# Optimization experiments

Measured on AMD Instinct MI355X. Metric: run time of the kernel, lower is better.

## Reference

```python
import jax, jax.numpy as jnp
import numpy as np

V, H, DEPTH = 32000, 512, 6
B, L = 8, 256
AD, TD = 1024, 1024
TA, TT = 200, 100
DI, DS, DC, DTR = 1024, 16, 4, 32  # d_inner=2*H, d_state, d_conv, dt_rank=ceil(H/16)


def causal_conv1d(x, w, b):
    # x: [B,L,DI], w: [DI,DC], b: [DI]; depthwise causal conv
    K = w.shape[1]
    xp = jnp.pad(x, ((0, 0), (K - 1, 0), (0, 0)))
    out = b
    for k in range(K):
        out = out + xp[:, k:k + x.shape[1], :] * w[:, k]
    return out


def layernorm(x, g, b, eps=1e-5):
    mu = jnp.mean(x, -1, keepdims=True)
    var = jnp.var(x, -1, keepdims=True)
    return (x - mu) * jax.lax.rsqrt(var + eps) * g + b


def mamba_block(x, ipw, cw, cb, xpw, dtw, dtb, Alog, Dp, ow):
    # x: [B,L,H]
    xz = x @ ipw.T                       # [B,L,2*DI]
    xin, z = jnp.split(xz, 2, axis=-1)
    xc = jax.nn.silu(causal_conv1d(xin, cw, cb))  # [B,L,DI]
    dbl = xc @ xpw.T                     # [B,L,DTR+2*DS]
    dt = jax.nn.softplus(dbl[..., :DTR] @ dtw.T + dtb)    # [B,L,DI]
    Bm = dbl[..., DTR:DTR + DS]          # [B,L,DS]
    Cm = dbl[..., DTR + DS:]             # [B,L,DS]
    A = -jnp.exp(Alog)                   # [DI,DS]
    dA = jnp.exp(dt[..., None] * A)                       # [B,L,DI,DS]
    dBu = dt[..., None] * Bm[:, :, None, :] * xc[..., None]

    def step(h, inp):
        dA_t, dBu_t, C_t = inp
        h = h * dA_t + dBu_t             # [B,DI,DS]
        return h, jnp.einsum('bds,bs->bd', h, C_t)

    h0 = jnp.zeros((x.shape[0], DI, DS), x.dtype)
    _, ys = jax.lax.scan(step, h0, (dA.transpose(1, 0, 2, 3),
                                    dBu.transpose(1, 0, 2, 3),
                                    Cm.transpose(1, 0, 2)))
    y = ys.transpose(1, 0, 2) + Dp * xc  # [B,L,DI]
    y = y * jax.nn.silu(z)
    return y @ ow.T                      # [B,L,H]


def setup_inputs() -> dict:
    key = jax.random.key(0)
    ks = jax.random.split(key, 32)
    f = jnp.float32
    s = 0.02
    inp = {
        'input_ids': jax.random.randint(ks[0], (B, L), 0, V),
        'audio_feats': jax.random.normal(ks[1], (B, TA, AD), f),
        'text_feats': jax.random.normal(ks[2], (B, TT, TD), f),
        'audio_mask': jnp.zeros((B, TA), bool),
        'text_mask': jnp.zeros((B, TT), bool),
        'tok_emb': jax.random.normal(ks[3], (V, H), f) * s,
        'pos_emb': jax.random.normal(ks[4], (1, L, H), f) * s,
        'audio_w': jax.random.normal(ks[5], (H, AD), f) * s,
        'audio_b': jnp.zeros((H,), f),
        'text_w': jax.random.normal(ks[6], (H, TD), f) * s,
        'text_b': jnp.zeros((H,), f),
        'mod_emb': jnp.zeros((2, H), f),
        'cond_w': jax.random.normal(ks[7], (H, H), f) * s,
        'cond_b': jnp.zeros((H,), f),
        'in_proj_w': jax.random.normal(ks[8], (DEPTH, 2 * DI, H), f) * s,
        'conv_w': jax.random.normal(ks[9], (DEPTH, DI, DC), f) * s,
        'conv_b': jnp.zeros((DEPTH, DI), f),
        'x_proj_w': jax.random.normal(ks[10], (DEPTH, DTR + 2 * DS, DI), f) * s,
        'dt_w': jax.random.normal(ks[11], (DEPTH, DI, DTR), f) * s,
        'dt_b': jnp.full((DEPTH, DI), -4.6, f),  # softplus(-4.6)~0.01, realistic dt init
        'A_log': jnp.broadcast_to(jnp.log(jnp.arange(1, DS + 1, dtype=f)), (DEPTH, DI, DS)) + 0.0,
        'D_skip': jnp.ones((DEPTH, DI), f),
        'out_w': jax.random.normal(ks[12], (DEPTH, H, DI), f) * s,
        'ln_g': jnp.ones((DEPTH, H), f),
        'ln_b': jnp.zeros((DEPTH, H), f),
        'head_w': jax.random.normal(ks[13], (V, H), f) * s,
        'head_b': jnp.zeros((V,), f),
    }
    return inp


def reference(input_ids, audio_feats, text_feats, audio_mask, text_mask,
              tok_emb, pos_emb, audio_w, audio_b, text_w, text_b, mod_emb,
              cond_w, cond_b, in_proj_w, conv_w, conv_b, x_proj_w, dt_w, dt_b,
              A_log, D_skip, out_w, ln_g, ln_b, head_w, head_b):
    x = tok_emb[input_ids] + pos_emb[:, :input_ids.shape[1], :]
    # build memory + pooled condition
    mem_a = audio_feats @ audio_w.T + audio_b + mod_emb[0]
    mem_t = text_feats @ text_w.T + text_b + mod_emb[1]
    memory = jnp.concatenate([mem_a, mem_t], axis=1)      # [B,TA+TT,H]
    mask = jnp.concatenate([audio_mask, text_mask], axis=1)
    valid = (~mask)[..., None].astype(memory.dtype)
    denom = jnp.maximum(valid.sum(axis=1), 1.0)
    pooled = (memory * valid).sum(axis=1) / denom
    cond = pooled @ cond_w.T + cond_b
    x = x + cond[:, None, :]
    for i in range(DEPTH):
        y = mamba_block(x, in_proj_w[i], conv_w[i], conv_b[i], x_proj_w[i],
                        dt_w[i], dt_b[i], A_log[i], D_skip[i], out_w[i])
        x = layernorm(x + y, ln_g[i], ln_b[i])
    return x @ head_w.T + head_b  # [B,L,V]
```

## Files before the change

### kernel.cpp

```cpp
#include <hip/hip_runtime.h>
#include <hip/hip_bf16.h>

#define V_    32000
#define H_    512
#define DEPTH_ 6
#define B_    8
#define L_    256
#define TA_   200
#define TT_   100
#define AD_   1024
#define DI_   1024
#define DS_   16
#define DTR_  32
#define M_    (B_*L_)

typedef __hip_bfloat16 bf16;
static __device__ __forceinline__ float b2f(bf16 x){ return __bfloat162float(x); }
static __device__ __forceinline__ float siluf(float x){ return x / (1.f + __expf(-x)); }

template<bool F32>
static __device__ __forceinline__ float ld(const void* p, size_t i){
    if (F32) return ((const float*)p)[i];
    else     return __bfloat162float(((const bf16*)p)[i]);
}

typedef __attribute__((ext_vector_type(8))) short s16x8;
typedef __attribute__((ext_vector_type(4))) float f32x4;

static __device__ __forceinline__ short f2bf_s(float f){
    union { bf16 b; short s; } u; u.b = __float2bfloat16(f); return u.s;
}
static __device__ __forceinline__ float bf_s2f(short s){
    union { bf16 b; short s2; } u; u.s2 = s; return __bfloat162float(u.b);
}
static __device__ __forceinline__ void split2(float f, short &h, short &l){
    h = f2bf_s(f);
    l = f2bf_s(f - bf_s2f(h));
}

__global__ void detect_kernel(const bf16* __restrict__ tok, int* __restrict__ flag){
    __shared__ int s;
    if (threadIdx.x==0) s = 0;
    __syncthreads();
    for (int i=threadIdx.x; i<4096; i+=256){
        float v = b2f(tok[i]);
        if (!(fabsf(v) < 1e3f)) atomicOr(&s, 1);
    }
    __syncthreads();
    if (threadIdx.x==0) *flag = s;
}

template<bool F32>
__global__ void feat_sum_kernel(const void* __restrict__ feats, const unsigned char* __restrict__ mask,
                                int T, float* __restrict__ out, const int* __restrict__ fl)
{
    if ((*fl!=0)!=F32) return;
    int d = blockIdx.x*256 + threadIdx.x;
    int b = blockIdx.y;
    const unsigned char* mb = mask + b*T;
    float s = 0.f;
    for (int t=0;t<T;t++) if (!mb[t]) s += ld<F32>(feats, (size_t)b*T*AD_ + (size_t)t*AD_ + d);
    out[b*AD_+d] = s;
}

__global__ void count_kernel(const unsigned char* __restrict__ am, const unsigned char* __restrict__ tm,
                             float* __restrict__ cnt )
{
    int i = threadIdx.x;
    if (i < B_)        { int c=0; for (int t=0;t<TA_;t++) c += am[i*TA_+t]?0:1; cnt[i] = (float)c; }
    else if (i < 2*B_) { int b=i-B_; int c=0; for (int t=0;t<TT_;t++) c += tm[b*TT_+t]?0:1; cnt[B_+b]=(float)c; }
}

template<bool F32>
__global__ __launch_bounds__(256) void pooled_kernel(const float* __restrict__ sa, const float* __restrict__ st,
    const float* __restrict__ cnt, const void* __restrict__ Wa, const void* __restrict__ ab,
    const void* __restrict__ Wt, const void* __restrict__ tb, const void* __restrict__ me,
    float* __restrict__ pooled, const int* __restrict__ fl)
{
    if ((*fl!=0)!=F32) return;
    int b = blockIdx.x;
    __shared__ float s_a[AD_], s_t[AD_];
    for (int i=threadIdx.x;i<AD_;i+=256){ s_a[i]=sa[b*AD_+i]; s_t[i]=st[b*AD_+i]; }
    __syncthreads();
    float ca = cnt[b], ct = cnt[B_+b];
    float denom = fmaxf(ca+ct, 1.0f);
    for (int h=threadIdx.x; h<H_; h+=256){
        float acc = 0.f;
        for (int k=0;k<AD_;k++) acc = fmaf(s_a[k], ld<F32>(Wa,(size_t)h*AD_+k), acc);
        for (int k=0;k<AD_;k++) acc = fmaf(s_t[k], ld<F32>(Wt,(size_t)h*AD_+k), acc);
        acc += ca*(ld<F32>(ab,h) + ld<F32>(me,h));
        acc += ct*(ld<F32>(tb,h) + ld<F32>(me,H_+h));
        pooled[b*H_+h] = acc/denom;
    }
}

template<bool F32>
__global__ __launch_bounds__(256) void cond_kernel(const float* __restrict__ pooled,
    const void* __restrict__ cw, const void* __restrict__ cb, float* __restrict__ cond,
    const int* __restrict__ fl)
{
    if ((*fl!=0)!=F32) return;
    int b = blockIdx.x;
    __shared__ float ps[H_];
    for (int i=threadIdx.x;i<H_;i+=256) ps[i]=pooled[b*H_+i];
    __syncthreads();
    for (int h=threadIdx.x; h<H_; h+=256){
        float acc = ld<F32>(cb,h);
        for (int k=0;k<H_;k++) acc = fmaf(ps[k], ld<F32>(cw,(size_t)h*H_+k), acc);
        cond[b*H_+h] = acc;
    }
}

template<bool F32>
__global__ void embed_kernel(const int* __restrict__ ids, const void* __restrict__ tok,
    const void* __restrict__ pos, const float* __restrict__ cond, float* __restrict__ x,
    const int* __restrict__ fl)
{
    if ((*fl!=0)!=F32) return;
    int tid = blockIdx.x*256 + threadIdx.x;
    if (tid >= M_*H_) return;
    int m = tid >> 9, h = tid & (H_-1);
    int b = m >> 8, l = m & (L_-1);
    x[tid] = ld<F32>(tok,(size_t)ids[m]*H_ + h) + ld<F32>(pos,(size_t)l*H_+h) + cond[b*H_+h];
}

template<bool F32>
__global__ __launch_bounds__(256) void gemm_kernel(const float* __restrict__ A, const void* __restrict__ Bw,
    float* __restrict__ Cf, void* __restrict__ Cb, const void* __restrict__ bias,
    int M, int N, int K, int MLOOP, const int* __restrict__ fl)
{
    if ((*fl!=0)!=F32) return;
    __shared__ short Ah[128][40];
    __shared__ short Al[128][40];
    __shared__ short Bh[128][40];
    __shared__ short Bl[128][40];

    const int tid = threadIdx.x;
    const int l    = tid & 63;
    const int wid  = tid >> 6;
    const int wr   = wid >> 1, wc = wid & 1;
    const int lrow = l & 15;
    const int lk   = (l >> 4) << 3;
    const int n0   = blockIdx.x * 128;

    for (int mt = 0; mt < MLOOP; ++mt){
        const int m0 = (blockIdx.y * MLOOP + mt) * 128;
        f32x4 acc[4][4] = {};

        for (int k0 = 0; k0 < K; k0 += 32){
            #pragma unroll
            for (int p=0;p<4;p++){
                int fidx = (p<<8) + tid;
                int row  = fidx >> 3;
                int kq   = (fidx & 7) << 2;
                float4 v = *(const float4*)(A + (size_t)(m0+row)*K + k0 + kq);
                short4 h, lo;
                split2(v.x, h.x, lo.x);
                split2(v.y, h.y, lo.y);
                split2(v.z, h.z, lo.z);
                split2(v.w, h.w, lo.w);
                *(short4*)&Ah[row][kq] = h;
                *(short4*)&Al[row][kq] = lo;
            }
            if (F32){
                #pragma unroll
                for (int p=0;p<4;p++){
                    int fidx = (p<<8) + tid;
                    int row  = fidx >> 3;
                    int kq   = (fidx & 7) << 2;
                    float4 v = *(const float4*)((const float*)Bw + (size_t)(n0+row)*K + k0 + kq);
                    short4 h, lo;
                    split2(v.x, h.x, lo.x);
                    split2(v.y, h.y, lo.y);
                    split2(v.z, h.z, lo.z);
                    split2(v.w, h.w, lo.w);
                    *(short4*)&Bh[row][kq] = h;
                    *(short4*)&Bl[row][kq] = lo;
                }
            } else {
                #pragma unroll
                for (int p=0;p<2;p++){
                    int fidx = (p<<8) + tid;
                    int row  = fidx >> 2;
                    int kq   = (fidx & 3) << 3;
                    s16x8 v = *(const s16x8*)((const short*)Bw + (size_t)(n0+row)*K + k0 + kq);
                    *(s16x8*)&Bh[row][kq] = v;
                }
            }
            __syncthreads();

            s16x8 fah[4], fal[4], fbh[4], fbl[4];
            #pragma unroll
            for (int i=0;i<4;i++){
                int ar = wr*64 + i*16 + lrow;
                fah[i] = *(const s16x8*)&Ah[ar][lk];
                fal[i] = *(const s16x8*)&Al[ar][lk];
                int br = wc*64 + i*16 + lrow;
                fbh[i] = *(const s16x8*)&Bh[br][lk];
                if (F32) fbl[i] = *(const s16x8*)&Bl[br][lk];
            }
            #pragma unroll
            for (int i=0;i<4;i++){
                #pragma unroll
                for (int j=0;j<4;j++){
                    acc[i][j] = __builtin_amdgcn_mfma_f32_16x16x32_bf16(fah[i], fbh[j], acc[i][j], 0,0,0);
                    acc[i][j] = __builtin_amdgcn_mfma_f32_16x16x32_bf16(fal[i], fbh[j], acc[i][j], 0,0,0);
                    if (F32)
                        acc[i][j] = __builtin_amdgcn_mfma_f32_16x16x32_bf16(fah[i], fbl[j], acc[i][j], 0,0,0);
                }
            }
            __syncthreads();
        }

        const int rbase = (l >> 4) << 2;
        #pragma unroll
        for (int i=0;i<4;i++){
            int mrow = m0 + wr*64 + i*16 + rbase;
            #pragma unroll
            for (int j=0;j<4;j++){
                int ncol = n0 + wc*64 + j*16 + lrow;
                float bv = bias ? ld<F32>(bias,(size_t)ncol) : 0.f;
                #pragma unroll
                for (int r=0;r<4;r++){
                    float outv = acc[i][j][r] + bv;
                    if (Cb){
                        if (F32) ((float*)Cb)[(size_t)(mrow+r)*N+ncol] = outv;
                        else     ((bf16*)Cb)[(size_t)(mrow+r)*N+ncol] = __float2bfloat16(outv);
                    } else {
                        Cf[(size_t)(mrow+r)*N+ncol] = outv;
                    }
                }
            }
        }
    }
}

template<bool F32>
__global__ void conv_silu_kernel(const float* __restrict__ xz, const void* __restrict__ cw,
                                 const void* __restrict__ cb, float* __restrict__ xc,
                                 const int* __restrict__ fl)
{
    if ((*fl!=0)!=F32) return;
    int tid = blockIdx.x*256 + threadIdx.x;
    if (tid >= M_*DI_) return;
    int m = tid >> 10, d = tid & (DI_-1);
    int l = m & (L_-1);
    float acc = ld<F32>(cb,d);
    #pragma unroll
    for (int k=0;k<4;k++){
        int l2 = l - 3 + k;
        if (l2 >= 0) acc = fmaf(xz[(size_t)(m-3+k)*(2*DI_) + d], ld<F32>(cw,(size_t)d*4+k), acc);
    }
    xc[tid] = siluf(acc);
}

template<bool F32>
__global__ __launch_bounds__(256) void xproj_kernel(const float* __restrict__ xc,
    const void* __restrict__ xpw, float* __restrict__ dbl, const int* __restrict__ fl)
{
    if ((*fl!=0)!=F32) return;
    int m = blockIdx.x;
    __shared__ float xs[DI_];
    __shared__ float part[64][5];
    for (int i=threadIdx.x;i<DI_;i+=256) xs[i] = xc[(size_t)m*DI_ + i];
    __syncthreads();
    int n = threadIdx.x & 63, c = threadIdx.x >> 6;
    const float* xv = xs + c*256;
    size_t wo = (size_t)n*DI_ + c*256;
    float acc = 0.f;
    for (int k=0;k<256;k++) acc = fmaf(xv[k], ld<F32>(xpw, wo+k), acc);
    part[n][c] = acc;
    __syncthreads();
    if (threadIdx.x < 64){
        dbl[(size_t)m*64 + threadIdx.x] = part[threadIdx.x][0]+part[threadIdx.x][1]
                                        + part[threadIdx.x][2]+part[threadIdx.x][3];
    }
}

template<bool F32>
__global__ __launch_bounds__(256) void dt_kernel(const float* __restrict__ dbl, const void* __restrict__ dtw,
    const void* __restrict__ dtb, float* __restrict__ dt, const int* __restrict__ fl)
{
    if ((*fl!=0)!=F32) return;
    int tid = blockIdx.x*256 + threadIdx.x;
    int m = tid >> 10;
    int d = tid & (DI_-1);
    __shared__ float ds_[DTR_];
    if (threadIdx.x < DTR_) ds_[threadIdx.x] = dbl[(size_t)m*64 + threadIdx.x];
    __syncthreads();
    float acc = ld<F32>(dtb,d);
    #pragma unroll
    for (int j=0;j<DTR_;j++) acc = fmaf(ds_[j], ld<F32>(dtw,(size_t)d*DTR_+j), acc);
    float sp = acc > 0.f ? acc + log1pf(__expf(-acc)) : log1pf(__expf(acc));
    dt[tid] = sp;
}

template<bool F32>
__global__ __launch_bounds__(256) void scan_kernel(const float* __restrict__ dt, const float* __restrict__ xc,
    const float* __restrict__ dbl, const float* __restrict__ xz,
    const void* __restrict__ Alog, const void* __restrict__ Dsk,
    float* __restrict__ ys, const int* __restrict__ fl)
{
    if ((*fl!=0)!=F32) return;
    int tid = threadIdx.x;
    int s = tid & 15, dloc = tid >> 4;
    int d = blockIdx.x*16 + dloc;
    int b = blockIdx.y;
    float aA = -__expf(ld<F32>(Alog,(size_t)d*DS_+s));
    float dp = ld<F32>(Dsk,d);
    float h = 0.f;
    int m0 = b*L_;
    float dtc = dt[(size_t)m0*DI_ + d];
    float xcc = xc[(size_t)m0*DI_ + d];
    float Bc  = dbl[(size_t)m0*64 + 32 + s];
    float Cc  = dbl[(size_t)m0*64 + 48 + s];
    for (int t=0;t<L_;t++){
        int m  = m0 + t;
        int mn = m + (t < L_-1 ? 1 : 0);
        float dtn = dt[(size_t)mn*DI_ + d];
        float xcn = xc[(size_t)mn*DI_ + d];
        float Bn  = dbl[(size_t)mn*64 + 32 + s];
        float Cn  = dbl[(size_t)mn*64 + 48 + s];
        float dA = __expf(dtc * aA);
        h = fmaf(h, dA, dtc*Bc*xcc);
        float p = h*Cc;
        p += __shfl_xor(p, 1, 16);
        p += __shfl_xor(p, 2, 16);
        p += __shfl_xor(p, 4, 16);
        p += __shfl_xor(p, 8, 16);
        if (s == 0){
            float zv = xz[(size_t)m*(2*DI_) + DI_ + d];
            ys[(size_t)m*DI_ + d] = (p + dp*xcc) * siluf(zv);
        }
        dtc=dtn; xcc=xcn; Bc=Bn; Cc=Cn;
    }
}

template<bool F32>
__global__ __launch_bounds__(256) void add_ln_kernel(float* __restrict__ x, const float* __restrict__ yp,
    const void* __restrict__ g, const void* __restrict__ bt, const int* __restrict__ fl)
{
    if ((*fl!=0)!=F32) return;
    int m = blockIdx.x;
    int tid = threadIdx.x;
    float r0 = x[(size_t)m*H_ + tid]       + yp[(size_t)m*H_ + tid];
    float r1 = x[(size_t)m*H_ + tid + 256] + yp[(size_t)m*H_ + tid + 256];
    float s = r0 + r1, q = r0*r0 + r1*r1;
    #pragma unroll
    for (int off=32; off>=1; off>>=1){ s += __shfl_xor(s, off, 64); q += __shfl_xor(q, off, 64); }
    __shared__ float ss[4], qq[4];
    int w = tid >> 6;
    if ((tid & 63)==0){ ss[w]=s; qq[w]=q; }
    __syncthreads();
    float S = ss[0]+ss[1]+ss[2]+ss[3];
    float Q = qq[0]+qq[1]+qq[2]+qq[3];
    float mean = S / (float)H_;
    float var  = Q / (float)H_ - mean*mean;
    float inv  = rsqrtf(var + 1e-5f);
    x[(size_t)m*H_+tid]       = (r0-mean)*inv*ld<F32>(g,tid)     + ld<F32>(bt,tid);
    x[(size_t)m*H_+tid+256]   = (r1-mean)*inv*ld<F32>(g,tid+256) + ld<F32>(bt,tid+256);
}

#define DUAL(kern, grid, block, ...) do { \
    kern<false><<<grid, block, 0, stream>>>(__VA_ARGS__); \
    kern<true><<<grid, block, 0, stream>>>(__VA_ARGS__); } while(0)

extern "C" void kernel_launch(void* const* d_in, const int* in_sizes, int n_in,
                              void* d_out, int out_size, void* d_ws, size_t ws_size,
                              hipStream_t stream)
{
    const int*  ids = (const int*)d_in[0];
    const void* af  = d_in[1];
    const void* tf  = d_in[2];
    const unsigned char* am = (const unsigned char*)d_in[3];
    const unsigned char* tm = (const unsigned char*)d_in[4];
    const void* tok = d_in[5];
    const void* pos = d_in[6];
    const void* aw  = d_in[7];
    const void* ab  = d_in[8];
    const void* tw  = d_in[9];
    const void* tbb = d_in[10];
    const void* me  = d_in[11];
    const void* cw  = d_in[12];
    const void* cb  = d_in[13];
    const void* ipw = d_in[14];
    const void* cvw = d_in[15];
    const void* cvb = d_in[16];
    const void* xpw = d_in[17];
    const void* dtw = d_in[18];
    const void* dtb = d_in[19];
    const void* Alg = d_in[20];
    const void* Dsk = d_in[21];
    const void* ow  = d_in[22];
    const void* lng = d_in[23];
    const void* lnb = d_in[24];
    const void* hw  = d_in[25];
    const void* hb  = d_in[26];

    float* ws   = (float*)d_ws;
    float* x    = ws;
    float* xz   = x    + (size_t)M_*H_;
    float* xc   = xz   + (size_t)M_*2*DI_;
    float* dbl  = xc   + (size_t)M_*DI_;
    float* dtv  = dbl  + (size_t)M_*64;
    float* ysb  = dtv  + (size_t)M_*DI_;
    float* ypj  = ysb  + (size_t)M_*DI_;
    float* sa   = ypj  + (size_t)M_*H_;
    float* st   = sa   + B_*AD_;
    float* cnt  = st   + B_*AD_;
    float* pooled = cnt + 2*B_;
    float* cond = pooled + B_*H_;
    int*   dflag = (int*)(cond + B_*H_);

    detect_kernel<<<1, 256, 0, stream>>>((const bf16*)tok, dflag);

    DUAL(feat_sum_kernel, dim3(AD_/256, B_), 256, af, am, TA_, sa, dflag);
    DUAL(feat_sum_kernel, dim3(AD_/256, B_), 256, tf, tm, TT_, st, dflag);
    count_kernel<<<1, 64, 0, stream>>>(am, tm, cnt);
    DUAL(pooled_kernel, B_, 256, sa, st, cnt, aw, ab, tw, tbb, me, pooled, dflag);
    DUAL(cond_kernel, B_, 256, pooled, cw, cb, cond, dflag);
    DUAL(embed_kernel, (M_*H_+255)/256, 256, ids, tok, pos, cond, x, dflag);

    for (int layer=0; layer<DEPTH_; ++layer){
        size_t o_ipw = (size_t)layer*2*DI_*H_;
        size_t o_cvw = (size_t)layer*DI_*4;
        size_t o_cvb = (size_t)layer*DI_;
        size_t o_xpw = (size_t)layer*64*DI_;
        size_t o_dtw = (size_t)layer*DI_*DTR_;
        size_t o_dtb = (size_t)layer*DI_;
        size_t o_alg = (size_t)layer*DI_*DS_;
        size_t o_dsk = (size_t)layer*DI_;
        size_t o_ow  = (size_t)layer*H_*DI_;
        size_t o_ln  = (size_t)layer*H_;
        const void* ipw_h = (const void*)((const bf16*)ipw + o_ipw);
        const void* ipw_f = (const void*)((const float*)ipw + o_ipw);
        const void* cvw_h = (const void*)((const bf16*)cvw + o_cvw);
        const void* cvw_f = (const void*)((const float*)cvw + o_cvw);
        const void* cvb_h = (const void*)((const bf16*)cvb + o_cvb);
        const void* cvb_f = (const void*)((const float*)cvb + o_cvb);
        const void* xpw_h = (const void*)((const bf16*)xpw + o_xpw);
        const void* xpw_f = (const void*)((const float*)xpw + o_xpw);
        const void* dtw_h = (const void*)((const bf16*)dtw + o_dtw);
        const void* dtw_f = (const void*)((const float*)dtw + o_dtw);
        const void* dtb_h = (const void*)((const bf16*)dtb + o_dtb);
        const void* dtb_f = (const void*)((const float*)dtb + o_dtb);
        const void* alg_h = (const void*)((const bf16*)Alg + o_alg);
        const void* alg_f = (const void*)((const float*)Alg + o_alg);
        const void* dsk_h = (const void*)((const bf16*)Dsk + o_dsk);
        const void* dsk_f = (const void*)((const float*)Dsk + o_dsk);
        const void* ow_h  = (const void*)((const bf16*)ow + o_ow);
        const void* ow_f  = (const void*)((const float*)ow + o_ow);
        const void* lng_h = (const void*)((const bf16*)lng + o_ln);
        const void* lng_f = (const void*)((const float*)lng + o_ln);
        const void* lnb_h = (const void*)((const bf16*)lnb + o_ln);
        const void* lnb_f = (const void*)((const float*)lnb + o_ln);

        gemm_kernel<false><<<dim3(2*DI_/128, M_/128), 256, 0, stream>>>(x, ipw_h, xz, nullptr, nullptr, M_, 2*DI_, H_, 1, dflag);
        gemm_kernel<true ><<<dim3(2*DI_/128, M_/128), 256, 0, stream>>>(x, ipw_f, xz, nullptr, nullptr, M_, 2*DI_, H_, 1, dflag);
        conv_silu_kernel<false><<<(M_*DI_+255)/256, 256, 0, stream>>>(xz, cvw_h, cvb_h, xc, dflag);
        conv_silu_kernel<true ><<<(M_*DI_+255)/256, 256, 0, stream>>>(xz, cvw_f, cvb_f, xc, dflag);
        xproj_kernel<false><<<M_, 256, 0, stream>>>(xc, xpw_h, dbl, dflag);
        xproj_kernel<true ><<<M_, 256, 0, stream>>>(xc, xpw_f, dbl, dflag);
        dt_kernel<false><<<M_*DI_/256, 256, 0, stream>>>(dbl, dtw_h, dtb_h, dtv, dflag);
        dt_kernel<true ><<<M_*DI_/256, 256, 0, stream>>>(dbl, dtw_f, dtb_f, dtv, dflag);
        scan_kernel<false><<<dim3(DI_/16, B_), 256, 0, stream>>>(dtv, xc, dbl, xz, alg_h, dsk_h, ysb, dflag);
        scan_kernel<true ><<<dim3(DI_/16, B_), 256, 0, stream>>>(dtv, xc, dbl, xz, alg_f, dsk_f, ysb, dflag);
        gemm_kernel<false><<<dim3(H_/128, M_/128), 256, 0, stream>>>(ysb, ow_h, ypj, nullptr, nullptr, M_, H_, DI_, 1, dflag);
        gemm_kernel<true ><<<dim3(H_/128, M_/128), 256, 0, stream>>>(ysb, ow_f, ypj, nullptr, nullptr, M_, H_, DI_, 1, dflag);
        add_ln_kernel<false><<<M_, 256, 0, stream>>>(x, ypj, lng_h, lnb_h, dflag);
        add_ln_kernel<true ><<<M_, 256, 0, stream>>>(x, ypj, lng_f, lnb_f, dflag);
    }

    DUAL(gemm_kernel, dim3(V_/128, M_/(128*8)), 256, x, hw, nullptr, d_out, hb, M_, V_, H_, 8, dflag);
}
```

Baseline: 3.305 ms.

## Pre-split activations into bf16 hi/lo, fuse conv/xproj/dt, nontemporal head stores

Producers (embed, add_ln, scan) now write the activations already split into bf16 high and low halves. The GEMMs load these directly instead of re-splitting fp32 A tiles for every output column block. The conv+silu, x_proj and dt/softplus kernels are merged into a single per-row mid kernel, which removes two launch pairs and the intermediate round trips. The final vocab-head GEMM uses nontemporal stores for its large output. In exchange, the hi/lo activation buffers take extra memory, the producers do more writes, and the shared memory for B-low is shrunk in the bf16 path.

```diff
diff --git a/kernel.cpp b/kernel.cpp
--- a/kernel.cpp
+++ b/kernel.cpp
@@ -114,26 +114,31 @@
 template<bool F32>
 __global__ void embed_kernel(const int* __restrict__ ids, const void* __restrict__ tok,
     const void* __restrict__ pos, const float* __restrict__ cond, float* __restrict__ x,
-    const int* __restrict__ fl)
+    short* __restrict__ xh, short* __restrict__ xl, const int* __restrict__ fl)
 {
     if ((*fl!=0)!=F32) return;
     int tid = blockIdx.x*256 + threadIdx.x;
     if (tid >= M_*H_) return;
     int m = tid >> 9, h = tid & (H_-1);
     int b = m >> 8, l = m & (L_-1);
-    x[tid] = ld<F32>(tok,(size_t)ids[m]*H_ + h) + ld<F32>(pos,(size_t)l*H_+h) + cond[b*H_+h];
-}
-
-template<bool F32>
-__global__ __launch_bounds__(256) void gemm_kernel(const float* __restrict__ A, const void* __restrict__ Bw,
+    float v = ld<F32>(tok,(size_t)ids[m]*H_ + h) + ld<F32>(pos,(size_t)l*H_+h) + cond[b*H_+h];
+    x[tid] = v;
+    short hh, ll; split2(v, hh, ll);
+    xh[tid] = hh; xl[tid] = ll;
+}
+
+template<bool F32>
+__global__ __launch_bounds__(256) void gemm_kernel(
+    const short* __restrict__ Ah, const short* __restrict__ Al,
+    const void* __restrict__ Bw,
     float* __restrict__ Cf, void* __restrict__ Cb, const void* __restrict__ bias,
-    int M, int N, int K, int MLOOP, const int* __restrict__ fl)
-{
-    if ((*fl!=0)!=F32) return;
-    __shared__ short Ah[128][40];
-    __shared__ short Al[128][40];
-    __shared__ short Bh[128][40];
-    __shared__ short Bl[128][40];
+    int M, int N, int K, int MLOOP, int NT, const int* __restrict__ fl)
+{
+    if ((*fl!=0)!=F32) return;
+    __shared__ short Ahs[128][40];
+    __shared__ short Als[128][40];
+    __shared__ short Bhs[128][40];
+    __shared__ short Bls[F32?128:1][40];
 
     const int tid = threadIdx.x;
     const int l    = tid & 63;
@@ -149,18 +154,12 @@
 
         for (int k0 = 0; k0 < K; k0 += 32){
             #pragma unroll
-            for (int p=0;p<4;p++){
+            for (int p=0;p<2;p++){
                 int fidx = (p<<8) + tid;
-                int row  = fidx >> 3;
-                int kq   = (fidx & 7) << 2;
-                float4 v = *(const float4*)(A + (size_t)(m0+row)*K + k0 + kq);
-                short4 h, lo;
-                split2(v.x, h.x, lo.x);
-                split2(v.y, h.y, lo.y);
-                split2(v.z, h.z, lo.z);
-                split2(v.w, h.w, lo.w);
-                *(short4*)&Ah[row][kq] = h;
-                *(short4*)&Al[row][kq] = lo;
+                int row  = fidx >> 2;
+                int kq   = (fidx & 3) << 3;
+                *(s16x8*)&Ahs[row][kq] = *(const s16x8*)(Ah + (size_t)(m0+row)*K + k0 + kq);
+                *(s16x8*)&Als[row][kq] = *(const s16x8*)(Al + (size_t)(m0+row)*K + k0 + kq);
             }
             if (F32){
                 #pragma unroll
@@ -174,8 +173,8 @@
                     split2(v.y, h.y, lo.y);
                     split2(v.z, h.z, lo.z);
                     split2(v.w, h.w, lo.w);
-                    *(short4*)&Bh[row][kq] = h;
-                    *(short4*)&Bl[row][kq] = lo;
+                    *(short4*)&Bhs[row][kq] = h;
+                    *(short4*)&Bls[row][kq] = lo;
                 }
             } else {
                 #pragma unroll
@@ -183,8 +182,7 @@
                     int fidx = (p<<8) + tid;
                     int row  = fidx >> 2;
                     int kq   = (fidx & 3) << 3;
-                    s16x8 v = *(const s16x8*)((const short*)Bw + (size_t)(n0+row)*K + k0 + kq);
-                    *(s16x8*)&Bh[row][kq] = v;
+                    *(s16x8*)&Bhs[row][kq] = *(const s16x8*)((const short*)Bw + (size_t)(n0+row)*K + k0 + kq);
                 }
             }
             __syncthreads();
@@ -193,11 +191,11 @@
             #pragma unroll
             for (int i=0;i<4;i++){
                 int ar = wr*64 + i*16 + lrow;
-                fah[i] = *(const s16x8*)&Ah[ar][lk];
-                fal[i] = *(const s16x8*)&Al[ar][lk];
+                fah[i] = *(const s16x8*)&Ahs[ar][lk];
+                fal[i] = *(const s16x8*)&Als[ar][lk];
                 int br = wc*64 + i*16 + lrow;
-                fbh[i] = *(const s16x8*)&Bh[br][lk];
-                if (F32) fbl[i] = *(const s16x8*)&Bl[br][lk];
+                fbh[i] = *(const s16x8*)&Bhs[br][lk];
+                if (F32) fbl[i] = *(const s16x8*)&Bls[br][lk];
             }
             #pragma unroll
             for (int i=0;i<4;i++){
@@ -224,8 +222,16 @@
                 for (int r=0;r<4;r++){
                     float outv = acc[i][j][r] + bv;
                     if (Cb){
-                        if (F32) ((float*)Cb)[(size_t)(mrow+r)*N+ncol] = outv;
-                        else     ((bf16*)Cb)[(size_t)(mrow+r)*N+ncol] = __float2bfloat16(outv);
+                        if (F32){
+                            float* pp = (float*)Cb + (size_t)(mrow+r)*N+ncol;
+                            if (NT) __builtin_nontemporal_store(outv, pp);
+                            else    *pp = outv;
+                        } else {
+                            short sv = f2bf_s(outv);
+                            short* pp = (short*)Cb + (size_t)(mrow+r)*N+ncol;
+                            if (NT) __builtin_nontemporal_store(sv, pp);
+                            else    *pp = sv;
+                        }
                     } else {
                         Cf[(size_t)(mrow+r)*N+ncol] = outv;
                     }
@@ -236,70 +242,65 @@
 }
 
 template<bool F32>
-__global__ void conv_silu_kernel(const float* __restrict__ xz, const void* __restrict__ cw,
-                                 const void* __restrict__ cb, float* __restrict__ xc,
-                                 const int* __restrict__ fl)
-{
-    if ((*fl!=0)!=F32) return;
-    int tid = blockIdx.x*256 + threadIdx.x;
-    if (tid >= M_*DI_) return;
-    int m = tid >> 10, d = tid & (DI_-1);
+__global__ __launch_bounds__(256) void mid_kernel(const float* __restrict__ xz,
+    const void* __restrict__ cw, const void* __restrict__ cb,
+    const void* __restrict__ xpw, const void* __restrict__ dtw, const void* __restrict__ dtb,
+    float* __restrict__ xc, float* __restrict__ dbl, float* __restrict__ dtv,
+    const int* __restrict__ fl)
+{
+    if ((*fl!=0)!=F32) return;
+    int m = blockIdx.x;
     int l = m & (L_-1);
-    float acc = ld<F32>(cb,d);
-    #pragma unroll
-    for (int k=0;k<4;k++){
-        int l2 = l - 3 + k;
-        if (l2 >= 0) acc = fmaf(xz[(size_t)(m-3+k)*(2*DI_) + d], ld<F32>(cw,(size_t)d*4+k), acc);
-    }
-    xc[tid] = siluf(acc);
-}
-
-template<bool F32>
-__global__ __launch_bounds__(256) void xproj_kernel(const float* __restrict__ xc,
-    const void* __restrict__ xpw, float* __restrict__ dbl, const int* __restrict__ fl)
-{
-    if ((*fl!=0)!=F32) return;
-    int m = blockIdx.x;
+    int tid = threadIdx.x;
     __shared__ float xs[DI_];
     __shared__ float part[64][5];
-    for (int i=threadIdx.x;i<DI_;i+=256) xs[i] = xc[(size_t)m*DI_ + i];
-    __syncthreads();
-    int n = threadIdx.x & 63, c = threadIdx.x >> 6;
+    __shared__ float ds_[DTR_];
+
+    #pragma unroll
+    for (int p=0;p<4;p++){
+        int d = tid + (p<<8);
+        float acc = ld<F32>(cb,d);
+        #pragma unroll
+        for (int k=0;k<4;k++){
+            int l2 = l - 3 + k;
+            if (l2 >= 0) acc = fmaf(xz[(size_t)(m-3+k)*(2*DI_) + d], ld<F32>(cw,(size_t)d*4+k), acc);
+        }
+        float v = siluf(acc);
+        xs[d] = v;
+        xc[(size_t)m*DI_ + d] = v;
+    }
+    __syncthreads();
+
+    int n = tid & 63, c = tid >> 6;
     const float* xv = xs + c*256;
     size_t wo = (size_t)n*DI_ + c*256;
     float acc = 0.f;
     for (int k=0;k<256;k++) acc = fmaf(xv[k], ld<F32>(xpw, wo+k), acc);
     part[n][c] = acc;
     __syncthreads();
-    if (threadIdx.x < 64){
-        dbl[(size_t)m*64 + threadIdx.x] = part[threadIdx.x][0]+part[threadIdx.x][1]
-                                        + part[threadIdx.x][2]+part[threadIdx.x][3];
-    }
-}
-
-template<bool F32>
-__global__ __launch_bounds__(256) void dt_kernel(const float* __restrict__ dbl, const void* __restrict__ dtw,
-    const void* __restrict__ dtb, float* __restrict__ dt, const int* __restrict__ fl)
-{
-    if ((*fl!=0)!=F32) return;
-    int tid = blockIdx.x*256 + threadIdx.x;
-    int m = tid >> 10;
-    int d = tid & (DI_-1);
-    __shared__ float ds_[DTR_];
-    if (threadIdx.x < DTR_) ds_[threadIdx.x] = dbl[(size_t)m*64 + threadIdx.x];
-    __syncthreads();
-    float acc = ld<F32>(dtb,d);
+    if (tid < 64){
+        float s = part[tid][0]+part[tid][1]+part[tid][2]+part[tid][3];
+        dbl[(size_t)m*64 + tid] = s;
+        if (tid < DTR_) ds_[tid] = s;
+    }
+    __syncthreads();
+
     #pragma unroll
-    for (int j=0;j<DTR_;j++) acc = fmaf(ds_[j], ld<F32>(dtw,(size_t)d*DTR_+j), acc);
-    float sp = acc > 0.f ? acc + log1pf(__expf(-acc)) : log1pf(__expf(acc));
-    dt[tid] = sp;
+    for (int p=0;p<4;p++){
+        int d = tid + (p<<8);
+        float a2 = ld<F32>(dtb,d);
+        #pragma unroll
+        for (int j=0;j<DTR_;j++) a2 = fmaf(ds_[j], ld<F32>(dtw,(size_t)d*DTR_+j), a2);
+        float sp = a2 > 0.f ? a2 + log1pf(__expf(-a2)) : log1pf(__expf(a2));
+        dtv[(size_t)m*DI_ + d] = sp;
+    }
 }
 
 template<bool F32>
 __global__ __launch_bounds__(256) void scan_kernel(const float* __restrict__ dt, const float* __restrict__ xc,
     const float* __restrict__ dbl, const float* __restrict__ xz,
     const void* __restrict__ Alog, const void* __restrict__ Dsk,
-    float* __restrict__ ys, const int* __restrict__ fl)
+    short* __restrict__ ysh, short* __restrict__ ysl, const int* __restrict__ fl)
 {
     if ((*fl!=0)!=F32) return;
     int tid = threadIdx.x;
@@ -330,7 +331,10 @@
         p += __shfl_xor(p, 8, 16);
         if (s == 0){
             float zv = xz[(size_t)m*(2*DI_) + DI_ + d];
-            ys[(size_t)m*DI_ + d] = (p + dp*xcc) * siluf(zv);
+            float yv = (p + dp*xcc) * siluf(zv);
+            short hh, ll; split2(yv, hh, ll);
+            ysh[(size_t)m*DI_ + d] = hh;
+            ysl[(size_t)m*DI_ + d] = ll;
         }
         dtc=dtn; xcc=xcn; Bc=Bn; Cc=Cn;
     }
@@ -338,7 +342,8 @@
 
 template<bool F32>
 __global__ __launch_bounds__(256) void add_ln_kernel(float* __restrict__ x, const float* __restrict__ yp,
-    const void* __restrict__ g, const void* __restrict__ bt, const int* __restrict__ fl)
+    const void* __restrict__ g, const void* __restrict__ bt,
+    short* __restrict__ xh, short* __restrict__ xl, const int* __restrict__ fl)
 {
     if ((*fl!=0)!=F32) return;
     int m = blockIdx.x;
@@ -357,8 +362,13 @@
     float mean = S / (float)H_;
     float var  = Q / (float)H_ - mean*mean;
     float inv  = rsqrtf(var + 1e-5f);
-    x[(size_t)m*H_+tid]       = (r0-mean)*inv*ld<F32>(g,tid)     + ld<F32>(bt,tid);
-    x[(size_t)m*H_+tid+256]   = (r1-mean)*inv*ld<F32>(g,tid+256) + ld<F32>(bt,tid+256);
+    float o0 = (r0-mean)*inv*ld<F32>(g,tid)     + ld<F32>(bt,tid);
+    float o1 = (r1-mean)*inv*ld<F32>(g,tid+256) + ld<F32>(bt,tid+256);
+    x[(size_t)m*H_+tid]     = o0;
+    x[(size_t)m*H_+tid+256] = o1;
+    short hh, ll;
+    split2(o0, hh, ll); xh[(size_t)m*H_+tid]     = hh; xl[(size_t)m*H_+tid]     = ll;
+    split2(o1, hh, ll); xh[(size_t)m*H_+tid+256] = hh; xl[(size_t)m*H_+tid+256] = ll;
 }
 
 #define DUAL(kern, grid, block, ...) do { \
@@ -410,7 +420,12 @@
     float* cnt  = st   + B_*AD_;
     float* pooled = cnt + 2*B_;
     float* cond = pooled + B_*H_;
-    int*   dflag = (int*)(cond + B_*H_);
+    short* xh   = (short*)(cond + B_*H_);
+    short* xl   = xh + (size_t)M_*H_;
+    int*   dflag = (int*)(xl + (size_t)M_*H_);
+
+    short* ysh  = (short*)ysb;
+    short* ysl  = ysh + (size_t)M_*DI_;
 
     detect_kernel<<<1, 256, 0, stream>>>((const bf16*)tok, dflag);
 
@@ -419,7 +434,7 @@
     count_kernel<<<1, 64, 0, stream>>>(am, tm, cnt);
     DUAL(pooled_kernel, B_, 256, sa, st, cnt, aw, ab, tw, tbb, me, pooled, dflag);
     DUAL(cond_kernel, B_, 256, pooled, cw, cb, cond, dflag);
-    DUAL(embed_kernel, (M_*H_+255)/256, 256, ids, tok, pos, cond, x, dflag);
+    DUAL(embed_kernel, (M_*H_+255)/256, 256, ids, tok, pos, cond, x, xh, xl, dflag);
 
     for (int layer=0; layer<DEPTH_; ++layer){
         size_t o_ipw = (size_t)layer*2*DI_*H_;
@@ -455,21 +470,17 @@
         const void* lnb_h = (const void*)((const bf16*)lnb + o_ln);
         const void* lnb_f = (const void*)((const float*)lnb + o_ln);
 
-        gemm_kernel<false><<<dim3(2*DI_/128, M_/128), 256, 0, stream>>>(x, ipw_h, xz, nullptr, nullptr, M_, 2*DI_, H_, 1, dflag);
-        gemm_kernel<true ><<<dim3(2*DI_/128, M_/128), 256, 0, stream>>>(x, ipw_f, xz, nullptr, nullptr, M_, 2*DI_, H_, 1, dflag);
-        conv_silu_kernel<false><<<(M_*DI_+255)/256, 256, 0, stream>>>(xz, cvw_h, cvb_h, xc, dflag);
-        conv_silu_kernel<true ><<<(M_*DI_+255)/256, 256, 0, stream>>>(xz, cvw_f, cvb_f, xc, dflag);
-        xproj_kernel<false><<<M_, 256, 0, stream>>>(xc, xpw_h, dbl, dflag);
-        xproj_kernel<true ><<<M_, 256, 0, stream>>>(xc, xpw_f, dbl, dflag);
-        dt_kernel<false><<<M_*DI_/256, 256, 0, stream>>>(dbl, dtw_h, dtb_h, dtv, dflag);
-        dt_kernel<true ><<<M_*DI_/256, 256, 0, stream>>>(dbl, dtw_f, dtb_f, dtv, dflag);
-        scan_kernel<false><<<dim3(DI_/16, B_), 256, 0, stream>>>(dtv, xc, dbl, xz, alg_h, dsk_h, ysb, dflag);
-        scan_kernel<true ><<<dim3(DI_/16, B_), 256, 0, stream>>>(dtv, xc, dbl, xz, alg_f, dsk_f, ysb, dflag);
-        gemm_kernel<false><<<dim3(H_/128, M_/128), 256, 0, stream>>>(ysb, ow_h, ypj, nullptr, nullptr, M_, H_, DI_, 1, dflag);
-        gemm_kernel<true ><<<dim3(H_/128, M_/128), 256, 0, stream>>>(ysb, ow_f, ypj, nullptr, nullptr, M_, H_, DI_, 1, dflag);
-        add_ln_kernel<false><<<M_, 256, 0, stream>>>(x, ypj, lng_h, lnb_h, dflag);
-        add_ln_kernel<true ><<<M_, 256, 0, stream>>>(x, ypj, lng_f, lnb_f, dflag);
-    }
-
-    DUAL(gemm_kernel, dim3(V_/128, M_/(128*8)), 256, x, hw, nullptr, d_out, hb, M_, V_, H_, 8, dflag);
-}
+        gemm_kernel<false><<<dim3(2*DI_/128, M_/128), 256, 0, stream>>>(xh, xl, ipw_h, xz, nullptr, nullptr, M_, 2*DI_, H_, 1, 0, dflag);
+        gemm_kernel<true ><<<dim3(2*DI_/128, M_/128), 256, 0, stream>>>(xh, xl, ipw_f, xz, nullptr, nullptr, M_, 2*DI_, H_, 1, 0, dflag);
+        mid_kernel<false><<<M_, 256, 0, stream>>>(xz, cvw_h, cvb_h, xpw_h, dtw_h, dtb_h, xc, dbl, dtv, dflag);
+        mid_kernel<true ><<<M_, 256, 0, stream>>>(xz, cvw_f, cvb_f, xpw_f, dtw_f, dtb_f, xc, dbl, dtv, dflag);
+        scan_kernel<false><<<dim3(DI_/16, B_), 256, 0, stream>>>(dtv, xc, dbl, xz, alg_h, dsk_h, ysh, ysl, dflag);
+        scan_kernel<true ><<<dim3(DI_/16, B_), 256, 0, stream>>>(dtv, xc, dbl, xz, alg_f, dsk_f, ysh, ysl, dflag);
+        gemm_kernel<false><<<dim3(H_/128, M_/128), 256, 0, stream>>>(ysh, ysl, ow_h, ypj, nullptr, nullptr, M_, H_, DI_, 1, 0, dflag);
+        gemm_kernel<true ><<<dim3(H_/128, M_/128), 256, 0, stream>>>(ysh, ysl, ow_f, ypj, nullptr, nullptr, M_, H_, DI_, 1, 0, dflag);
+        add_ln_kernel<false><<<M_, 256, 0, stream>>>(x, ypj, lng_h, lnb_h, xh, xl, dflag);
+        add_ln_kernel<true ><<<M_, 256, 0, stream>>>(x, ypj, lng_f, lnb_f, xh, xl, dflag);
+    }
+
+    DUAL(gemm_kernel, dim3(V_/128, M_/(128*8)), 256, xh, xl, hw, nullptr, d_out, hb, M_, V_, H_, 8, 1, dflag);
+}
```

Measured after the change: 3.315 ms. No clear change (+0.3%).
